# Kernel tuning notes

Measured on AMD Instinct MI355X. Metric: run time of the kernel, lower is better.

The kernel has to match this reference:

```python
import jax, jax.numpy as jnp
import numpy as np

BS, LS, NWRD, D, H, NTGT, MC = 32, 512, 100000, 128, 512, 2048, 20
TEMP = 0.5  # gumbel-softmax temperature (self.last_t)
HLOSS_COEF = 0.03


def setup_inputs() -> dict:
    key = jax.random.key(0)
    ks = jax.random.split(key, 12)
    inp_word = jax.random.randint(ks[0], (BS, LS), 0, NWRD, dtype=jnp.int32)
    inp_char = jax.random.randint(ks[1], (BS, LS, MC), 0, 95, dtype=jnp.int32)
    inp_pos = jax.random.randint(ks[2], (BS, LS), 0, 50, dtype=jnp.int32)
    keyword_table = jax.random.bernoulli(ks[3], 0.1, (NWRD,))  # wid in keywords_set
    tgt_ids = jax.random.randint(ks[4], (NTGT,), 0, NWRD, dtype=jnp.int32)
    lut = jax.random.randint(ks[5], (NWRD, MC), 0, 95, dtype=jnp.int32)
    u = jax.random.uniform(ks[6], (BS, LS, NTGT), minval=1e-6, maxval=1.0 - 1e-6)
    gumbel = -jnp.log(-jnp.log(u))  # standard Gumbel(0,1) noise
    W = jax.random.normal(ks[7], (NWRD, D), dtype=jnp.float32) * 0.02
    W1 = jax.random.normal(ks[8], (D, H), dtype=jnp.float32) * (1.0 / np.sqrt(D))
    b1 = jnp.zeros((H,), jnp.float32)
    W2 = jax.random.normal(ks[9], (H, NTGT), dtype=jnp.float32) * (1.0 / np.sqrt(H))
    b2 = jnp.zeros((NTGT,), jnp.float32)
    return dict(inp_word=inp_word, inp_char=inp_char, inp_pos=inp_pos,
                keyword_table=keyword_table, tgt_ids=tgt_ids, lut=lut,
                gumbel=gumbel, W=W, W1=W1, b1=b1, W2=W2, b2=b2)


def reference(inp_word, inp_char, inp_pos, keyword_table, tgt_ids, lut,
              gumbel, W, W1, b1, W2, b2):
    # keyword membership mask (idx in the original; torch gathers only masked
    # spots -- here we compute densely and select with the mask, same math at
    # every masked position, identity elsewhere)
    mask = keyword_table[inp_word]                      # [bs, ls] bool

    x = W[inp_word]                                     # embed: [bs, ls, d]
    hdn = jax.nn.relu(jnp.einsum('bsd,dh->bsh', x, W1) + b1)
    logits = jnp.einsum('bsh,ht->bst', hdn, W2) + b2    # [bs, ls, ntgt]

    # log_p.masked_scatter_(idx, x.max(-1)[0])
    log_p = jnp.where(mask, logits.max(axis=-1), 0.0)

    # hloss: mean entropy over masked spots * 0.03
    lsm = jax.nn.log_softmax(logits, axis=-1)
    ent = -jnp.sum(jnp.exp(lsm) * lsm, axis=-1)         # [bs, ls]
    n_spots = jnp.maximum(mask.sum(), 1)
    loss_h = (ent * mask).sum() / n_spots * HLOSS_COEF

    # gumbel_softmax(x, t): softmax((logits + g) / t)
    sft = jax.nn.softmax((logits + gumbel) / TEMP, axis=-1)  # [bs, ls, ntgt]

    # hard pick mapped through tgtwords, scattered into word
    y = tgt_ids[jnp.argmax(sft, axis=-1)]               # [bs, ls]
    word = jnp.where(mask, y, inp_word)

    # soft embedding: sft @ word_emb_tgt, word_emb_tgt = W[tgt_ids]
    x_emb = jnp.einsum('bst,td->bsd', sft, W[tgt_ids])  # [bs, ls, d]
    word_emb = jnp.where(mask[..., None], x_emb, x)     # scatter into W[word]

    char = lut[word]                                    # word_to_char lookup

    return (mask.astype(jnp.float32), log_p, word, char, word_emb, loss_h)
```

## Files before the change

kernel.cpp:

```cpp
#include <hip/hip_runtime.h>
#include <cstdint>

#define R_TOT 16384
#define T_NT  2048
#define DD    128
#define HH    512
#define MC_   20
#define BR    32
#define STEPS 64
#define NBLK  (R_TOT / BR)

#define MASK_OFF 0
#define LOGP_OFF 16384
#define WORD_OFF 32768
#define CHAR_OFF 49152
#define EMB_OFF  376832
#define LOSS_OFF 2473984

#define X_OFF     0
#define HDN_OFF   2097152
#define HDNB_OFF  10485760
#define WT_OFF    14680064
#define WTT4_OFF  14942208
#define W2T_OFF   15204352
#define W2P_OFF   16252928
#define ENT_OFF   16777216
#define CNT_OFF   16777728

typedef __attribute__((ext_vector_type(8))) short short8v;
typedef __attribute__((ext_vector_type(4))) float f32x4;
typedef unsigned short ushort_t;

__device__ __forceinline__ ushort_t f2bf(float f) {
    union { float f; unsigned int u; } v; v.f = f;
    unsigned int r = v.u + 0x7FFFu + ((v.u >> 16) & 1u);
    return (ushort_t)(r >> 16);
}

__device__ __forceinline__ void stage16(const ushort_t* gsrc, ushort_t* ldst) {
    __builtin_amdgcn_global_load_lds(
        (const __attribute__((address_space(1))) unsigned int*)gsrc,
        (__attribute__((address_space(3))) unsigned int*)ldst, 16, 0, 0);
}

__global__ __launch_bounds__(256) void k1_gather(
    const int* __restrict__ inp_word, const int* __restrict__ tgt_ids,
    const float* __restrict__ W, float* __restrict__ x, float* __restrict__ wtgt)
{
    int row = blockIdx.x * 2 + (threadIdx.x >> 7);
    int d = threadIdx.x & 127;
    if (row < R_TOT) {
        int wsrc = inp_word[row];
        x[(size_t)row * DD + d] = W[(size_t)wsrc * DD + d];
    } else {
        int rr = row - R_TOT;
        if (rr < T_NT) {
            int wsrc = tgt_ids[rr];
            wtgt[(size_t)rr * DD + d] = W[(size_t)wsrc * DD + d];
        }
    }
}

__global__ __launch_bounds__(256) void k1b_wtgtT4(
    const float* __restrict__ wtgt, ushort_t* __restrict__ wtgtT4)
{
    const int js = blockIdx.x, t = threadIdx.x;
    #pragma unroll
    for (int i = 0; i < 4; ++i) {
        int s = i * 256 + t;
        int cs = s >> 9, rem = s & 511;
        int df = rem >> 6, lane = rem & 63;
        int lrow = lane & 15, kg = lane >> 4;
        ushort_t* dst = wtgtT4 + (size_t)(((js * 2 + cs) * 8 + df) * 512 + lane * 8);
        #pragma unroll
        for (int j = 0; j < 8; ++j) {
            dst[j] = (j < 4)
                ? f2bf(wtgt[(size_t)(js * 32 + cs * 16 + kg * 4 + j) * DD + df * 16 + lrow])
                : (ushort_t)0;
        }
    }
}

__global__ __launch_bounds__(256) void k0_w2t(
    const float* __restrict__ W2, float* __restrict__ W2Tf, ushort_t* __restrict__ W2p)
{
    __shared__ float tile[32][33];
    const int js = blockIdx.x, ks = blockIdx.y;
    const int cb = js * 32, kb = ks * 32;
    const int lx = threadIdx.x & 31, ly = threadIdx.x >> 5;
    #pragma unroll
    for (int i = 0; i < 32; i += 8)
        tile[ly + i][lx] = W2[(size_t)(kb + ly + i) * T_NT + cb + lx];
    __syncthreads();
    #pragma unroll
    for (int i = 0; i < 32; i += 8) {
        int c = cb + ly + i, k = kb + lx;
        W2Tf[(size_t)c * HH + k] = tile[lx][ly + i];
    }
    if (threadIdx.x < 128) {
        int c = threadIdx.x >> 2, kgrp = threadIdx.x & 3;
        ushort_t* dst = W2p + (size_t)((js * 16 + ks) * 1024 + (c * 4 + kgrp) * 8);
        #pragma unroll
        for (int i = 0; i < 8; ++i)
            dst[i] = f2bf(tile[kgrp * 8 + i][c]);
    }
}

__global__ __launch_bounds__(256) void k2_hdn(
    const float* __restrict__ x, const float* __restrict__ W1,
    const float* __restrict__ b1, float* __restrict__ hdn, ushort_t* __restrict__ hdnB)
{
    __shared__ float As[16][64];
    __shared__ float Bs[16][64];
    const int t = threadIdx.x;
    const int bm = blockIdx.x * 64;
    const int bn = blockIdx.y * 64;
    const int tx = t & 15, ty = t >> 4;
    float acc[4][4] = {};
    for (int k0 = 0; k0 < DD; k0 += 16) {
        {
            int m = t >> 2, kq = t & 3;
            float4 v = *(const float4*)(x + (size_t)(bm + m) * DD + k0 + kq * 4);
            As[kq * 4 + 0][m] = v.x; As[kq * 4 + 1][m] = v.y;
            As[kq * 4 + 2][m] = v.z; As[kq * 4 + 3][m] = v.w;
        }
        {
            int k = t >> 4, nq = t & 15;
            *(float4*)(&Bs[k][nq * 4]) =
                *(const float4*)(W1 + (size_t)(k0 + k) * HH + bn + nq * 4);
        }
        __syncthreads();
        #pragma unroll
        for (int k = 0; k < 16; ++k) {
            float a[4], b[4];
            #pragma unroll
            for (int i = 0; i < 4; i++) a[i] = As[k][ty * 4 + i];
            #pragma unroll
            for (int j = 0; j < 4; j++) b[j] = Bs[k][tx * 4 + j];
            #pragma unroll
            for (int i = 0; i < 4; i++)
                #pragma unroll
                for (int j = 0; j < 4; j++)
                    acc[i][j] = fmaf(a[i], b[j], acc[i][j]);
        }
        __syncthreads();
    }
    #pragma unroll
    for (int i = 0; i < 4; i++) {
        int m = bm + ty * 4 + i;
        int n = bn + tx * 4;
        float4 v;
        v.x = fmaxf(acc[i][0] + b1[n + 0], 0.f);
        v.y = fmaxf(acc[i][1] + b1[n + 1], 0.f);
        v.z = fmaxf(acc[i][2] + b1[n + 2], 0.f);
        v.w = fmaxf(acc[i][3] + b1[n + 3], 0.f);
        *(float4*)(hdn + (size_t)m * HH + n) = v;
        ushort4 hb;
        hb.x = f2bf(v.x); hb.y = f2bf(v.y); hb.z = f2bf(v.z); hb.w = f2bf(v.w);
        *(ushort4*)(hdnB + (size_t)m * HH + n) = hb;
    }
}

__global__ __launch_bounds__(256) void k3_fused(
    const ushort_t* __restrict__ hdnB, const float* __restrict__ hdn,
    const ushort_t* __restrict__ W2p, const float* __restrict__ W2Tf,
    const float* __restrict__ b2, const float* __restrict__ gumbel,
    const int* __restrict__ inp_word, const int* __restrict__ keyword_table,
    const int* __restrict__ tgt_ids, const int* __restrict__ lut,
    const float* __restrict__ x, const ushort_t* __restrict__ wtgtT4,
    float* __restrict__ out, float* __restrict__ entP, float* __restrict__ cntP)
{
    __shared__ ushort_t wS[2 * 16384];
    __shared__ float pS[4][16 * 20];
    __shared__ float statC1[2 * 16 * 8];
    __shared__ int   candS[BR * 2];
    __shared__ float invs2S[BR], entS[BR];
    __shared__ int   mskS[BR];

    const int t = threadIdx.x;
    const int wid = t >> 6, lane = t & 63;
    const int Mgrp = wid >> 1, Cgrp = wid & 1;
    const int lrow = lane & 15, kgrp = lane >> 4;
    const int row0 = blockIdx.x * BR;
    const int rowA = row0 + Mgrp * 16 + lrow;

    short8v av[16];
    #pragma unroll
    for (int ks = 0; ks < 16; ++ks)
        av[ks] = *(const short8v*)(hdnB + (size_t)rowA * HH + ks * 32 + kgrp * 8);

    const ushort_t* wb = wS + ((Cgrp * 16 + lrow) * 4 + kgrp) * 8;

    const float* gp0 = gumbel + (size_t)(row0 + Mgrp * 16 + kgrp * 4 + 0) * T_NT + Cgrp * 16 + lrow;
    const float* gp1 = gp0 + T_NT;
    const float* gp2 = gp1 + T_NT;
    const float* gp3 = gp2 + T_NT;
    const float* b2p = b2 + Cgrp * 16 + lrow;
    const ushort_t* vtp = wtgtT4 + (size_t)Cgrp * 4096 + lane * 8;

    float* pw = &pS[wid][0];

    float m_[4], sE_[4], sEl_[4], s2_[4], a1_[4], a2_[4];
    int i1_[4], i2_[4];
    #pragma unroll
    for (int q = 0; q < 4; ++q) {
        m_[q] = -1e30f; sE_[q] = 0.f; sEl_[q] = 0.f; s2_[q] = 0.f;
        a1_[q] = -1e30f; a2_[q] = -1e30f; i1_[q] = 0; i2_[q] = 0;
    }
    f32x4 accpv[8];
    #pragma unroll
    for (int df = 0; df < 8; ++df) accpv[df] = (f32x4){0.f, 0.f, 0.f, 0.f};

    {
        const ushort_t* src = W2p + t * 8;
        ushort_t* dst = wS + t * 8;
        #pragma unroll
        for (int i = 0; i < 8; ++i) stage16(src + i * 2048, dst + i * 2048);
    }
    __syncthreads();

    int colv = Cgrp * 16 + lrow;

    for (int s = 0; s < STEPS; ++s) {
        const int buf = s & 1;

        if (s + 1 < STEPS) {
            const ushort_t* src = W2p + (size_t)(s + 1) * 16384 + t * 8;
            ushort_t* dst = wS + (buf ^ 1) * 16384 + t * 8;
            #pragma unroll
            for (int i = 0; i < 8; ++i) stage16(src + i * 2048, dst + i * 2048);
        }

        float g0 = *gp0, g1 = *gp1, g2 = *gp2, g3 = *gp3;
        gp0 += 32; gp1 += 32; gp2 += 32; gp3 += 32;
        float b2v = *b2p; b2p += 32;
        short8v bvf[8];
        #pragma unroll
        for (int df = 0; df < 8; ++df)
            bvf[df] = *(const short8v*)(vtp + df * 512);
        vtp += 8192;

        const ushort_t* wbb = wb + buf * 16384;
        f32x4 ac0 = (f32x4){0.f,0.f,0.f,0.f}, ac1 = ac0, ac2 = ac0, ac3 = ac0;
        #pragma unroll
        for (int ks = 0; ks < 16; ks += 4) {
            ac0 = __builtin_amdgcn_mfma_f32_16x16x32_bf16(av[ks+0], *(const short8v*)(wbb + (ks+0)*1024), ac0, 0, 0, 0);
            ac1 = __builtin_amdgcn_mfma_f32_16x16x32_bf16(av[ks+1], *(const short8v*)(wbb + (ks+1)*1024), ac1, 0, 0, 0);
            ac2 = __builtin_amdgcn_mfma_f32_16x16x32_bf16(av[ks+2], *(const short8v*)(wbb + (ks+2)*1024), ac2, 0, 0, 0);
            ac3 = __builtin_amdgcn_mfma_f32_16x16x32_bf16(av[ks+3], *(const short8v*)(wbb + (ks+3)*1024), ac3, 0, 0, 0);
        }
        f32x4 acc = (ac0 + ac1) + (ac2 + ac3);

        float g4[4] = {g0, g1, g2, g3};
        #pragma unroll
        for (int q = 0; q < 4; ++q) {
            float l = acc[q] + b2v;
            m_[q] = fmaxf(m_[q], l);
            float e1 = __expf(l);
            sE_[q] += e1; sEl_[q] = fmaf(e1, l, sEl_[q]);
            float a = l + g4[q];
            float p = __expf(2.0f * a);
            s2_[q] += p;
            if (a > a1_[q]) { a2_[q] = a1_[q]; i2_[q] = i1_[q]; a1_[q] = a; i1_[q] = colv; }
            else if (a > a2_[q]) { a2_[q] = a; i2_[q] = colv; }
            pw[(kgrp * 4 + q) * 20 + lrow] = p;
        }

        {
            float4 p4 = *(const float4*)(pw + lrow * 20 + kgrp * 4);
            short8v pav;
            pav[0] = (short)f2bf(p4.x); pav[1] = (short)f2bf(p4.y);
            pav[2] = (short)f2bf(p4.z); pav[3] = (short)f2bf(p4.w);
            pav[4] = 0; pav[5] = 0; pav[6] = 0; pav[7] = 0;
            #pragma unroll
            for (int df = 0; df < 8; ++df)
                accpv[df] = __builtin_amdgcn_mfma_f32_16x16x32_bf16(pav, bvf[df], accpv[df], 0, 0, 0);
        }

        __syncthreads();
        colv += 32;
    }

    #pragma unroll
    for (int q = 0; q < 4; ++q) {
        #pragma unroll
        for (int mk = 1; mk < 16; mk <<= 1) {
            m_[q] = fmaxf(m_[q], __shfl_xor(m_[q], mk));
            sE_[q] += __shfl_xor(sE_[q], mk);
            sEl_[q] += __shfl_xor(sEl_[q], mk);
            s2_[q] += __shfl_xor(s2_[q], mk);
            float ob1 = __shfl_xor(a1_[q], mk); int oj1 = __shfl_xor(i1_[q], mk);
            float ob2 = __shfl_xor(a2_[q], mk); int oj2 = __shfl_xor(i2_[q], mk);
            if (ob1 > a1_[q] || (ob1 == a1_[q] && oj1 < i1_[q])) {
                if (a1_[q] > ob2 || (a1_[q] == ob2 && i1_[q] < oj2)) { a2_[q] = a1_[q]; i2_[q] = i1_[q]; }
                else { a2_[q] = ob2; i2_[q] = oj2; }
                a1_[q] = ob1; i1_[q] = oj1;
            } else {
                if (ob1 > a2_[q]) { a2_[q] = ob1; i2_[q] = oj1; }
            }
        }
    }

    if (Cgrp == 1 && lrow == 0) {
        #pragma unroll
        for (int q = 0; q < 4; ++q) {
            float* st = &statC1[(Mgrp * 16 + kgrp * 4 + q) * 8];
            st[0] = m_[q]; st[1] = sE_[q]; st[2] = sEl_[q]; st[3] = s2_[q];
            st[4] = a1_[q]; st[5] = __int_as_float(i1_[q]);
            st[6] = a2_[q]; st[7] = __int_as_float(i2_[q]);
        }
    }
    float* scr = (float*)wS;
    if (Cgrp == 1) {
        #pragma unroll
        for (int df = 0; df < 8; ++df)
            #pragma unroll
            for (int q = 0; q < 4; ++q)
                scr[Mgrp * 2048 + (kgrp * 4 + q) * 128 + df * 16 + lrow] = accpv[df][q];
    }
    __syncthreads();

    if (Cgrp == 0) {
        #pragma unroll
        for (int q = 0; q < 4; ++q) {
            int r = kgrp * 4 + q;
            const float* st = &statC1[(Mgrp * 16 + r) * 8];
            float bm = st[0], bsE = st[1], bsEl = st[2], bs2 = st[3];
            float ob1 = st[4]; int oj1 = __float_as_int(st[5]);
            float ob2 = st[6]; int oj2 = __float_as_int(st[7]);
            float m = fmaxf(m_[q], bm);
            float sE = sE_[q] + bsE, sEl = sEl_[q] + bsEl, s2 = s2_[q] + bs2;
            float a1 = a1_[q], a2 = a2_[q]; int i1 = i1_[q], i2 = i2_[q];
            if (ob1 > a1 || (ob1 == a1 && oj1 < i1)) {
                if (a1 > ob2 || (a1 == ob2 && i1 < oj2)) { a2 = a1; i2 = i1; }
                else { a2 = ob2; i2 = oj2; }
                a1 = ob1; i1 = oj1;
            } else {
                if (ob1 > a2) { a2 = ob1; i2 = oj1; }
            }
            if (lrow == 0) {
                int rl = Mgrp * 16 + r;
                int grow = row0 + rl;
                int w_in = inp_word[grow];
                int msk = keyword_table[w_in] != 0;
                out[MASK_OFF + grow] = msk ? 1.0f : 0.0f;
                out[LOGP_OFF + grow] = msk ? m : 0.0f;
                invs2S[rl] = 1.0f / s2;
                mskS[rl] = msk;
                entS[rl] = msk ? (__logf(sE) - sEl / sE) : 0.0f;
                candS[rl * 2 + 0] = i1;
                candS[rl * 2 + 1] = i2;
            }
        }
        #pragma unroll
        for (int df = 0; df < 8; ++df)
            #pragma unroll
            for (int q = 0; q < 4; ++q)
                accpv[df][q] += scr[Mgrp * 2048 + (kgrp * 4 + q) * 128 + df * 16 + lrow];
    }
    __syncthreads();

    if (Cgrp == 0) {
        #pragma unroll
        for (int df = 0; df < 8; ++df) {
            #pragma unroll
            for (int q = 0; q < 4; ++q) {
                int rl = Mgrp * 16 + kgrp * 4 + q;
                int grow = row0 + rl;
                int d = df * 16 + lrow;
                float val = accpv[df][q] * invs2S[rl];
                if (!mskS[rl]) val = x[(size_t)grow * DD + d];
                out[EMB_OFF + (size_t)grow * DD + d] = val;
            }
        }
    }

    for (int rr = wid; rr < BR; rr += 4) {
        int grow = row0 + rr;
        int i1 = candS[rr * 2 + 0], i2 = candS[rr * 2 + 1];
        const float* hrow = hdn + (size_t)grow * HH;
        float4 h0 = *(const float4*)(hrow + lane * 8);
        float4 h1 = *(const float4*)(hrow + lane * 8 + 4);
        float v1, v2;
        {
            const float* wrow = W2Tf + (size_t)i1 * HH;
            float4 w0 = *(const float4*)(wrow + lane * 8);
            float4 w1 = *(const float4*)(wrow + lane * 8 + 4);
            float sdot = h0.x*w0.x + h0.y*w0.y + h0.z*w0.z + h0.w*w0.w
                       + h1.x*w1.x + h1.y*w1.y + h1.z*w1.z + h1.w*w1.w;
            #pragma unroll
            for (int mk = 1; mk < 64; mk <<= 1) sdot += __shfl_xor(sdot, mk);
            v1 = sdot + b2[i1] + gumbel[(size_t)grow * T_NT + i1];
        }
        {
            const float* wrow = W2Tf + (size_t)i2 * HH;
            float4 w0 = *(const float4*)(wrow + lane * 8);
            float4 w1 = *(const float4*)(wrow + lane * 8 + 4);
            float sdot = h0.x*w0.x + h0.y*w0.y + h0.z*w0.z + h0.w*w0.w
                       + h1.x*w1.x + h1.y*w1.y + h1.z*w1.z + h1.w*w1.w;
            #pragma unroll
            for (int mk = 1; mk < 64; mk <<= 1) sdot += __shfl_xor(sdot, mk);
            v2 = sdot + b2[i2] + gumbel[(size_t)grow * T_NT + i2];
        }
        int ibest = (v2 > v1 || (v2 == v1 && i2 < i1)) ? i2 : i1;
        int w_in = inp_word[grow];
        int msk = mskS[rr];
        int word = msk ? tgt_ids[ibest] : w_in;
        if (lane == 0) out[WORD_OFF + grow] = (float)word;
        if (lane < MC_)
            out[CHAR_OFF + (size_t)grow * MC_ + lane] = (float)lut[(size_t)word * MC_ + lane];
    }

    if (t == 0) {
        float es = 0.f; int cs = 0;
        #pragma unroll
        for (int r = 0; r < BR; r++) { es += entS[r]; cs += mskS[r]; }
        entP[blockIdx.x] = es;
        cntP[blockIdx.x] = (float)cs;
    }
}

__global__ __launch_bounds__(256) void k4_loss(
    const float* __restrict__ entP, const float* __restrict__ cntP, float* __restrict__ out)
{
    __shared__ float sE[256], sC[256];
    int t = threadIdx.x;
    float e = 0.f, c = 0.f;
    for (int i = t; i < NBLK; i += 256) { e += entP[i]; c += cntP[i]; }
    sE[t] = e; sC[t] = c;
    __syncthreads();
    for (int s = 128; s > 0; s >>= 1) {
        if (t < s) { sE[t] += sE[t + s]; sC[t] += sC[t + s]; }
        __syncthreads();
    }
    if (t == 0) {
        float ns = fmaxf(sC[0], 1.0f);
        out[LOSS_OFF] = 0.03f * sE[0] / ns;
    }
}

extern "C" void kernel_launch(void* const* d_in, const int* in_sizes, int n_in,
                              void* d_out, int out_size, void* d_ws, size_t ws_size,
                              hipStream_t stream) {
    const int* inp_word = (const int*)d_in[0];
    const int* keyword_table = (const int*)d_in[3];
    const int* tgt_ids = (const int*)d_in[4];
    const int* lut = (const int*)d_in[5];
    const float* gumbel = (const float*)d_in[6];
    const float* W = (const float*)d_in[7];
    const float* W1 = (const float*)d_in[8];
    const float* b1 = (const float*)d_in[9];
    const float* W2 = (const float*)d_in[10];
    const float* b2 = (const float*)d_in[11];
    float* out = (float*)d_out;

    float* wsf = (float*)d_ws;
    float* x = wsf + X_OFF;
    float* hdn = wsf + HDN_OFF;
    ushort_t* hdnB = (ushort_t*)(wsf + HDNB_OFF);
    float* wtgt = wsf + WT_OFF;
    ushort_t* wtgtT4 = (ushort_t*)(wsf + WTT4_OFF);
    float* W2Tf = wsf + W2T_OFF;
    ushort_t* W2p = (ushort_t*)(wsf + W2P_OFF);
    float* entP = wsf + ENT_OFF;
    float* cntP = wsf + CNT_OFF;

    k1_gather<<<(R_TOT + T_NT) / 2, 256, 0, stream>>>(inp_word, tgt_ids, W, x, wtgt);
    k1b_wtgtT4<<<64, 256, 0, stream>>>(wtgt, wtgtT4);
    k0_w2t<<<dim3(T_NT / 32, HH / 32), 256, 0, stream>>>(W2, W2Tf, W2p);
    k2_hdn<<<dim3(R_TOT / 64, HH / 64), 256, 0, stream>>>(x, W1, b1, hdn, hdnB);
    k3_fused<<<NBLK, 256, 0, stream>>>(hdnB, hdn, W2p, W2Tf, b2, gumbel,
                                       inp_word, keyword_table, tgt_ids, lut,
                                       x, wtgtT4, out, entP, cntP);
    k4_loss<<<1, 256, 0, stream>>>(entP, cntP, out);
}
```

Baseline: 215.8 us.

## Swap MFMA operands so logits land row-major per lane, removing LDS transpose

Measured after the change: 206.2 us. -4.5%, faster.

```diff
diff --git a/kernel.cpp b/kernel.cpp
--- a/kernel.cpp
+++ b/kernel.cpp
@@ -171,8 +171,7 @@
     float* __restrict__ out, float* __restrict__ entP, float* __restrict__ cntP)
 {
     __shared__ ushort_t wS[2 * 16384];
-    __shared__ float pS[4][16 * 20];
-    __shared__ float statC1[2 * 16 * 8];
+    __shared__ float statC1[32 * 8];
     __shared__ int   candS[BR * 2];
     __shared__ float invs2S[BR], entS[BR];
     __shared__ int   mskS[BR];
@@ -191,22 +190,13 @@
 
     const ushort_t* wb = wS + ((Cgrp * 16 + lrow) * 4 + kgrp) * 8;
 
-    const float* gp0 = gumbel + (size_t)(row0 + Mgrp * 16 + kgrp * 4 + 0) * T_NT + Cgrp * 16 + lrow;
-    const float* gp1 = gp0 + T_NT;
-    const float* gp2 = gp1 + T_NT;
-    const float* gp3 = gp2 + T_NT;
-    const float* b2p = b2 + Cgrp * 16 + lrow;
+    const float* gp = gumbel + (size_t)rowA * T_NT + Cgrp * 16 + kgrp * 4;
+    const float* b2p = b2 + Cgrp * 16 + kgrp * 4;
     const ushort_t* vtp = wtgtT4 + (size_t)Cgrp * 4096 + lane * 8;
 
-    float* pw = &pS[wid][0];
-
-    float m_[4], sE_[4], sEl_[4], s2_[4], a1_[4], a2_[4];
-    int i1_[4], i2_[4];
-    #pragma unroll
-    for (int q = 0; q < 4; ++q) {
-        m_[q] = -1e30f; sE_[q] = 0.f; sEl_[q] = 0.f; s2_[q] = 0.f;
-        a1_[q] = -1e30f; a2_[q] = -1e30f; i1_[q] = 0; i2_[q] = 0;
-    }
+    float m_ = -1e30f, sE_ = 0.f, sEl_ = 0.f, s2_ = 0.f;
+    float a1_ = -1e30f, a2_ = -1e30f;
+    int i1_ = 0, i2_ = 0;
     f32x4 accpv[8];
     #pragma unroll
     for (int df = 0; df < 8; ++df) accpv[df] = (f32x4){0.f, 0.f, 0.f, 0.f};
@@ -217,9 +207,11 @@
         #pragma unroll
         for (int i = 0; i < 8; ++i) stage16(src + i * 2048, dst + i * 2048);
     }
+    float4 g4 = *(const float4*)gp;
+    float4 b2v4 = *(const float4*)b2p;
     __syncthreads();
 
-    int colv = Cgrp * 16 + lrow;
+    int c0 = Cgrp * 16 + kgrp * 4;
 
     for (int s = 0; s < STEPS; ++s) {
         const int buf = s & 1;
@@ -230,10 +222,10 @@
             #pragma unroll
             for (int i = 0; i < 8; ++i) stage16(src + i * 2048, dst + i * 2048);
         }
-
-        float g0 = *gp0, g1 = *gp1, g2 = *gp2, g3 = *gp3;
-        gp0 += 32; gp1 += 32; gp2 += 32; gp3 += 32;
-        float b2v = *b2p; b2p += 32;
+        const int adv = (s + 1 < STEPS) ? 32 : 0;
+        float4 gn4 = *(const float4*)(gp + adv);
+        float4 b2n4 = *(const float4*)(b2p + adv);
+        gp += 32; b2p += 32;
         short8v bvf[8];
         #pragma unroll
         for (int df = 0; df < 8; ++df)
@@ -244,71 +236,59 @@
         f32x4 ac0 = (f32x4){0.f,0.f,0.f,0.f}, ac1 = ac0, ac2 = ac0, ac3 = ac0;
         #pragma unroll
         for (int ks = 0; ks < 16; ks += 4) {
-            ac0 = __builtin_amdgcn_mfma_f32_16x16x32_bf16(av[ks+0], *(const short8v*)(wbb + (ks+0)*1024), ac0, 0, 0, 0);
-            ac1 = __builtin_amdgcn_mfma_f32_16x16x32_bf16(av[ks+1], *(const short8v*)(wbb + (ks+1)*1024), ac1, 0, 0, 0);
-            ac2 = __builtin_amdgcn_mfma_f32_16x16x32_bf16(av[ks+2], *(const short8v*)(wbb + (ks+2)*1024), ac2, 0, 0, 0);
-            ac3 = __builtin_amdgcn_mfma_f32_16x16x32_bf16(av[ks+3], *(const short8v*)(wbb + (ks+3)*1024), ac3, 0, 0, 0);
+            ac0 = __builtin_amdgcn_mfma_f32_16x16x32_bf16(*(const short8v*)(wbb + (ks+0)*1024), av[ks+0], ac0, 0, 0, 0);
+            ac1 = __builtin_amdgcn_mfma_f32_16x16x32_bf16(*(const short8v*)(wbb + (ks+1)*1024), av[ks+1], ac1, 0, 0, 0);
+            ac2 = __builtin_amdgcn_mfma_f32_16x16x32_bf16(*(const short8v*)(wbb + (ks+2)*1024), av[ks+2], ac2, 0, 0, 0);
+            ac3 = __builtin_amdgcn_mfma_f32_16x16x32_bf16(*(const short8v*)(wbb + (ks+3)*1024), av[ks+3], ac3, 0, 0, 0);
         }
         f32x4 acc = (ac0 + ac1) + (ac2 + ac3);
 
-        float g4[4] = {g0, g1, g2, g3};
+        short8v pav;
+        pav[4] = 0; pav[5] = 0; pav[6] = 0; pav[7] = 0;
         #pragma unroll
         for (int q = 0; q < 4; ++q) {
-            float l = acc[q] + b2v;
-            m_[q] = fmaxf(m_[q], l);
+            float l = acc[q] + b2v4[q];
+            m_ = fmaxf(m_, l);
             float e1 = __expf(l);
-            sE_[q] += e1; sEl_[q] = fmaf(e1, l, sEl_[q]);
+            sE_ += e1; sEl_ = fmaf(e1, l, sEl_);
             float a = l + g4[q];
             float p = __expf(2.0f * a);
-            s2_[q] += p;
-            if (a > a1_[q]) { a2_[q] = a1_[q]; i2_[q] = i1_[q]; a1_[q] = a; i1_[q] = colv; }
-            else if (a > a2_[q]) { a2_[q] = a; i2_[q] = colv; }
-            pw[(kgrp * 4 + q) * 20 + lrow] = p;
-        }
-
-        {
-            float4 p4 = *(const float4*)(pw + lrow * 20 + kgrp * 4);
-            short8v pav;
-            pav[0] = (short)f2bf(p4.x); pav[1] = (short)f2bf(p4.y);
-            pav[2] = (short)f2bf(p4.z); pav[3] = (short)f2bf(p4.w);
-            pav[4] = 0; pav[5] = 0; pav[6] = 0; pav[7] = 0;
-            #pragma unroll
-            for (int df = 0; df < 8; ++df)
-                accpv[df] = __builtin_amdgcn_mfma_f32_16x16x32_bf16(pav, bvf[df], accpv[df], 0, 0, 0);
-        }
-
+            s2_ += p;
+            if (a > a1_) { a2_ = a1_; i2_ = i1_; a1_ = a; i1_ = c0 + q; }
+            else if (a > a2_) { a2_ = a; i2_ = c0 + q; }
+            pav[q] = (short)f2bf(p);
+        }
+
+        #pragma unroll
+        for (int df = 0; df < 8; ++df)
+            accpv[df] = __builtin_amdgcn_mfma_f32_16x16x32_bf16(pav, bvf[df], accpv[df], 0, 0, 0);
+
+        g4 = gn4; b2v4 = b2n4; c0 += 32;
         __syncthreads();
-        colv += 32;
-    }
-
-    #pragma unroll
-    for (int q = 0; q < 4; ++q) {
-        #pragma unroll
-        for (int mk = 1; mk < 16; mk <<= 1) {
-            m_[q] = fmaxf(m_[q], __shfl_xor(m_[q], mk));
-            sE_[q] += __shfl_xor(sE_[q], mk);
-            sEl_[q] += __shfl_xor(sEl_[q], mk);
-            s2_[q] += __shfl_xor(s2_[q], mk);
-            float ob1 = __shfl_xor(a1_[q], mk); int oj1 = __shfl_xor(i1_[q], mk);
-            float ob2 = __shfl_xor(a2_[q], mk); int oj2 = __shfl_xor(i2_[q], mk);
-            if (ob1 > a1_[q] || (ob1 == a1_[q] && oj1 < i1_[q])) {
-                if (a1_[q] > ob2 || (a1_[q] == ob2 && i1_[q] < oj2)) { a2_[q] = a1_[q]; i2_[q] = i1_[q]; }
-                else { a2_[q] = ob2; i2_[q] = oj2; }
-                a1_[q] = ob1; i1_[q] = oj1;
-            } else {
-                if (ob1 > a2_[q]) { a2_[q] = ob1; i2_[q] = oj1; }
-            }
-        }
-    }
-
-    if (Cgrp == 1 && lrow == 0) {
-        #pragma unroll
-        for (int q = 0; q < 4; ++q) {
-            float* st = &statC1[(Mgrp * 16 + kgrp * 4 + q) * 8];
-            st[0] = m_[q]; st[1] = sE_[q]; st[2] = sEl_[q]; st[3] = s2_[q];
-            st[4] = a1_[q]; st[5] = __int_as_float(i1_[q]);
-            st[6] = a2_[q]; st[7] = __int_as_float(i2_[q]);
-        }
+    }
+
+    #pragma unroll
+    for (int mk = 16; mk < 64; mk <<= 1) {
+        m_ = fmaxf(m_, __shfl_xor(m_, mk));
+        sE_ += __shfl_xor(sE_, mk);
+        sEl_ += __shfl_xor(sEl_, mk);
+        s2_ += __shfl_xor(s2_, mk);
+        float ob1 = __shfl_xor(a1_, mk); int oj1 = __shfl_xor(i1_, mk);
+        float ob2 = __shfl_xor(a2_, mk); int oj2 = __shfl_xor(i2_, mk);
+        if (ob1 > a1_ || (ob1 == a1_ && oj1 < i1_)) {
+            if (a1_ > ob2 || (a1_ == ob2 && i1_ < oj2)) { a2_ = a1_; i2_ = i1_; }
+            else { a2_ = ob2; i2_ = oj2; }
+            a1_ = ob1; i1_ = oj1;
+        } else {
+            if (ob1 > a2_) { a2_ = ob1; i2_ = oj1; }
+        }
+    }
+
+    if (Cgrp == 1 && lane < 16) {
+        float* st = &statC1[(Mgrp * 16 + lane) * 8];
+        st[0] = m_; st[1] = sE_; st[2] = sEl_; st[3] = s2_;
+        st[4] = a1_; st[5] = __int_as_float(i1_);
+        st[6] = a2_; st[7] = __int_as_float(i2_);
     }
     float* scr = (float*)wS;
     if (Cgrp == 1) {
@@ -321,16 +301,14 @@
     __syncthreads();
 
     if (Cgrp == 0) {
-        #pragma unroll
-        for (int q = 0; q < 4; ++q) {
-            int r = kgrp * 4 + q;
-            const float* st = &statC1[(Mgrp * 16 + r) * 8];
+        if (lane < 16) {
+            const float* st = &statC1[(Mgrp * 16 + lane) * 8];
             float bm = st[0], bsE = st[1], bsEl = st[2], bs2 = st[3];
             float ob1 = st[4]; int oj1 = __float_as_int(st[5]);
             float ob2 = st[6]; int oj2 = __float_as_int(st[7]);
-            float m = fmaxf(m_[q], bm);
-            float sE = sE_[q] + bsE, sEl = sEl_[q] + bsEl, s2 = s2_[q] + bs2;
-            float a1 = a1_[q], a2 = a2_[q]; int i1 = i1_[q], i2 = i2_[q];
+            float m = fmaxf(m_, bm);
+            float sE = sE_ + bsE, sEl = sEl_ + bsEl, s2 = s2_ + bs2;
+            float a1 = a1_, a2 = a2_; int i1 = i1_, i2 = i2_;
             if (ob1 > a1 || (ob1 == a1 && oj1 < i1)) {
                 if (a1 > ob2 || (a1 == ob2 && i1 < oj2)) { a2 = a1; i2 = i1; }
                 else { a2 = ob2; i2 = oj2; }
@@ -338,19 +316,17 @@
             } else {
                 if (ob1 > a2) { a2 = ob1; i2 = oj1; }
             }
-            if (lrow == 0) {
-                int rl = Mgrp * 16 + r;
-                int grow = row0 + rl;
-                int w_in = inp_word[grow];
-                int msk = keyword_table[w_in] != 0;
-                out[MASK_OFF + grow] = msk ? 1.0f : 0.0f;
-                out[LOGP_OFF + grow] = msk ? m : 0.0f;
-                invs2S[rl] = 1.0f / s2;
-                mskS[rl] = msk;
-                entS[rl] = msk ? (__logf(sE) - sEl / sE) : 0.0f;
-                candS[rl * 2 + 0] = i1;
-                candS[rl * 2 + 1] = i2;
-            }
+            int rl = Mgrp * 16 + lane;
+            int grow = row0 + rl;
+            int w_in = inp_word[grow];
+            int msk = keyword_table[w_in] != 0;
+            out[MASK_OFF + grow] = msk ? 1.0f : 0.0f;
+            out[LOGP_OFF + grow] = msk ? m : 0.0f;
+            invs2S[rl] = 1.0f / s2;
+            mskS[rl] = msk;
+            entS[rl] = msk ? (__logf(sE) - sEl / sE) : 0.0f;
+            candS[rl * 2 + 0] = i1;
+            candS[rl * 2 + 1] = i2;
         }
         #pragma unroll
         for (int df = 0; df < 8; ++df)
```
